# Kernel optimization log

Hardware: AMD Instinct MI355X
Metric: run time of the kernel (lower is better)

Reference implementation:

```python
import jax, jax.numpy as jnp
import numpy as np

B, S, D, H = 2, 2048, 1024, 16
HD = D // H  # head_dim = 64


def setup_inputs() -> dict:
    key = jax.random.key(0)
    ks = jax.random.split(key, 5)
    scale = 1.0 / np.sqrt(D)
    return {
        "x": jax.random.normal(ks[0], (B, S, D), dtype=jnp.float32),
        "attention_mask": jnp.zeros((B, 1, 1, S), dtype=jnp.float32),
        "Wq": jax.random.normal(ks[1], (D, D), dtype=jnp.float32) * scale,
        "Wk": jax.random.normal(ks[2], (D, D), dtype=jnp.float32) * scale,
        "Wv": jax.random.normal(ks[3], (D, D), dtype=jnp.float32) * scale,
        "Wo": jax.random.normal(ks[4], (D, D), dtype=jnp.float32) * scale,
    }


def reference(x, attention_mask, Wq, Wk, Wv, Wo):
    # nn.Linear applies x @ W.T; weights here stored as [out, in]
    q = jnp.einsum("bsd,ed->bse", x, Wq).reshape(B, S, H, HD).transpose(0, 2, 1, 3)
    k = jnp.einsum("bsd,ed->bse", x, Wk).reshape(B, S, H, HD).transpose(0, 2, 1, 3)
    v = jnp.einsum("bsd,ed->bse", x, Wv).reshape(B, S, H, HD).transpose(0, 2, 1, 3)
    scores = jnp.einsum("bhqd,bhkd->bhqk", q, k) / jnp.sqrt(jnp.float32(HD))
    scores = scores + attention_mask  # additive mask, broadcasts [B,1,1,S]
    attn = jax.nn.softmax(scores, axis=-1)  # dropout p=0 (eval) -> identity
    ctx = jnp.einsum("bhqk,bhkd->bhqd", attn, v)
    ctx = ctx.transpose(0, 2, 1, 3).reshape(B, S, D)
    out = jnp.einsum("bsd,ed->bse", ctx, Wo)
    return out
```

## Files before the change

kernel.cpp:

```cpp
#include <hip/hip_runtime.h>
#include <hip/hip_bf16.h>
#include <cstdint>
#include <cstddef>


#define B_  2
#define S_  2048
#define D_  1024
#define H_  16
#define HD_ 64

typedef __bf16 bf16x8 __attribute__((ext_vector_type(8)));
typedef __bf16 bf16x4 __attribute__((ext_vector_type(4)));
typedef float  f32x4  __attribute__((ext_vector_type(4)));

__device__ __forceinline__ void async16(const __bf16* g, const __bf16* l) {
  __builtin_amdgcn_global_load_lds(
      (const __attribute__((address_space(1))) void*)(uintptr_t)g,
      (__attribute__((address_space(3))) void*)(uint32_t)(uintptr_t)l,
      16, 0, 0);
}

__global__ __launch_bounds__(256) void cvt_all(const float* __restrict__ x,
    const float* __restrict__ wq, const float* __restrict__ wk,
    const float* __restrict__ wv, const float* __restrict__ wo,
    __bf16* __restrict__ xb, __bf16* __restrict__ wqb, __bf16* __restrict__ wkb,
    __bf16* __restrict__ wvb, __bf16* __restrict__ wob) {
  const int sel = blockIdx.y;
  const float* src; __bf16* dst; int n;
  if      (sel == 0) { src = x;  dst = xb;  n = B_ * S_ * D_; }
  else if (sel == 1) { src = wq; dst = wqb; n = D_ * D_; }
  else if (sel == 2) { src = wk; dst = wkb; n = D_ * D_; }
  else if (sel == 3) { src = wv; dst = wvb; n = D_ * D_; }
  else               { src = wo; dst = wob; n = D_ * D_; }
  for (int i = blockIdx.x * 256 + threadIdx.x; i * 4 < n; i += gridDim.x * 256) {
    const float4 v = *(const float4*)(src + (size_t)i * 4);
    bf16x4 o;
    o[0] = (__bf16)v.x; o[1] = (__bf16)v.y; o[2] = (__bf16)v.z; o[3] = (__bf16)v.w;
    *(bf16x4*)(dst + (size_t)i * 4) = o;
  }
}

template <typename TC>
__device__ __forceinline__ void gemm97_body(const __bf16* __restrict__ A,
                                            const __bf16* __restrict__ Bm,
                                            TC* __restrict__ C,
                                            const int m0, const int n0,
                                            const int N, const int K) {
  __shared__ __align__(16) __bf16 As[128 * 64];
  __shared__ __align__(16) __bf16 Bs[128 * 64];
  const int tid  = threadIdx.x, lane = tid & 63, wave = tid >> 6;
  const int l15  = lane & 15,   quad = lane >> 4;
  const int wr   = wave >> 1,   wc   = wave & 1;
  const int ebase = wave * 2048 + lane * 8;

  f32x4 acc[4][4] = {};
  for (int k0 = 0; k0 < K; k0 += 64) {
#pragma unroll
    for (int i = 0; i < 4; ++i) {
      const int e = ebase + i * 512;
      const int row = e >> 6, col = e & 63;
      async16(A  + (size_t)(m0 + row) * K + k0 + col, As + (wave * 4 + i) * 512);
      async16(Bm + (size_t)(n0 + row) * K + k0 + col, Bs + (wave * 4 + i) * 512);
    }
    __syncthreads();
#pragma unroll
    for (int kk = 0; kk < 2; ++kk) {
      bf16x8 af[4], bfv[4];
#pragma unroll
      for (int rt = 0; rt < 4; ++rt)
        af[rt] = *(const bf16x8*)(As + (wr * 64 + rt * 16 + l15) * 64 + kk * 32 + quad * 8);
#pragma unroll
      for (int ct = 0; ct < 4; ++ct)
        bfv[ct] = *(const bf16x8*)(Bs + (wc * 64 + ct * 16 + l15) * 64 + kk * 32 + quad * 8);
#pragma unroll
      for (int rt = 0; rt < 4; ++rt)
#pragma unroll
        for (int ct = 0; ct < 4; ++ct)
          acc[rt][ct] = __builtin_amdgcn_mfma_f32_16x16x32_bf16(af[rt], bfv[ct], acc[rt][ct], 0, 0, 0);
    }
    __syncthreads();
  }
#pragma unroll
  for (int rt = 0; rt < 4; ++rt)
#pragma unroll
    for (int ct = 0; ct < 4; ++ct)
#pragma unroll
      for (int r = 0; r < 4; ++r) {
        const int row = m0 + wr * 64 + rt * 16 + quad * 4 + r;
        const int col = n0 + wc * 64 + ct * 16 + l15;
        C[(size_t)row * N + col] = (TC)acc[rt][ct][r];
      }
}

__global__ __launch_bounds__(256) void qkv_gemm(const __bf16* __restrict__ xb,
                                                const __bf16* __restrict__ wq,
                                                const __bf16* __restrict__ wk,
                                                const __bf16* __restrict__ wv,
                                                __bf16* __restrict__ qkv) {
  const int sel = blockIdx.x >> 3;
  const __bf16* Bm = (sel == 0) ? wq : (sel == 1) ? wk : wv;
  __bf16* C = qkv + (size_t)sel * ((size_t)B_ * S_ * D_);
  gemm97_body<__bf16>(xb, Bm, C, blockIdx.y * 128, (blockIdx.x & 7) * 128, D_, D_);
}

__global__ __launch_bounds__(256) void o_gemm(const __bf16* __restrict__ cb,
                                              const __bf16* __restrict__ wo,
                                              float* __restrict__ out) {
  gemm97_body<float>(cb, wo, out, blockIdx.y * 128, blockIdx.x * 128, D_, D_);
}

__global__ __launch_bounds__(256) void vtrans(const __bf16* __restrict__ vb,
                                              __bf16* __restrict__ vt) {
  __shared__ __bf16 tbuf[64][72];
  const int tid = threadIdx.x;
  const int s0 = blockIdx.x * 64, bh = blockIdx.y;
  const int b = bh >> 4, h = bh & 15;
  const __bf16* src = vb + ((size_t)b * S_ + s0) * D_ + h * HD_;
#pragma unroll
  for (int i = 0; i < 2; ++i) {
    const int r = i * 32 + (tid >> 3), c8 = (tid & 7) * 8;
    *(bf16x8*)(&tbuf[r][c8]) = *(const bf16x8*)(src + (size_t)r * D_ + c8);
  }
  __syncthreads();
  __bf16* dst = vt + (size_t)bh * HD_ * S_ + s0;
#pragma unroll
  for (int i = 0; i < 2; ++i) {
    const int hd = i * 32 + (tid >> 3), sc = (tid & 7) * 8;
    bf16x8 v;
#pragma unroll
    for (int j = 0; j < 8; ++j) v[j] = tbuf[sc + j][hd];
    *(bf16x8*)(dst + (size_t)hd * S_ + sc) = v;
  }
}

__global__ __launch_bounds__(256) void attn2(const __bf16* __restrict__ Q,
                                             const __bf16* __restrict__ K,
                                             const __bf16* __restrict__ Vt,
                                             const float* __restrict__ mask,
                                             __bf16* __restrict__ O) {
  constexpr int LKT = 72, LVT = 136, LPS = 136;
  __shared__ __align__(16) __bf16 kt[128 * LKT];
  __shared__ __align__(16) __bf16 vt[64 * LVT];
  __shared__ __align__(16) __bf16 ps[128 * LPS];
  __shared__ __align__(16) float  msk[128];

  const int tid  = threadIdx.x, lane = tid & 63, wave = tid >> 6;
  const int l15  = lane & 15,   quad = lane >> 4;
  const int b = blockIdx.z, h = blockIdx.y, q0 = blockIdx.x * 128;
  const size_t base   = (size_t)b * S_ * D_ + h * HD_;
  const size_t vtbase = (size_t)(b * H_ + h) * HD_ * S_;
  const int qw = q0 + wave * 32;

  bf16x8 qf[2][2];
#pragma unroll
  for (int t = 0; t < 2; ++t)
#pragma unroll
    for (int kb = 0; kb < 2; ++kb)
      qf[t][kb] = *(const bf16x8*)(Q + base + (size_t)(qw + t * 16 + l15) * D_ + kb * 32 + quad * 8);

  float m_run[2] = {-1e30f, -1e30f}, l_run[2] = {0.f, 0.f};
  f32x4 oacc[2][4] = {};

  for (int t0 = 0; t0 < S_; t0 += 128) {
    __syncthreads();
#pragma unroll
    for (int i = 0; i < 4; ++i) {
      const int idx = i * 256 + tid;
      { const int row = idx >> 3, c8 = (idx & 7) * 8;
        *(bf16x8*)(kt + row * LKT + c8) =
            *(const bf16x8*)(K + base + (size_t)(t0 + row) * D_ + c8); }
      { const int row = idx >> 4, c8 = (idx & 15) * 8;
        *(bf16x8*)(vt + row * LVT + c8) =
            *(const bf16x8*)(Vt + vtbase + (size_t)row * S_ + t0 + c8); }
    }
    if (tid < 128) msk[tid] = mask[(size_t)b * S_ + t0 + tid];
    __syncthreads();

    f32x4 sacc[8][2] = {};
#pragma unroll
    for (int kti = 0; kti < 8; ++kti) {
      const __bf16* kr = kt + (kti * 16 + l15) * LKT + quad * 8;
      const bf16x8 a0 = *(const bf16x8*)(kr);
      const bf16x8 a1 = *(const bf16x8*)(kr + 32);
#pragma unroll
      for (int t = 0; t < 2; ++t) {
        sacc[kti][t] = __builtin_amdgcn_mfma_f32_16x16x32_bf16(a0, qf[t][0], sacc[kti][t], 0, 0, 0);
        sacc[kti][t] = __builtin_amdgcn_mfma_f32_16x16x32_bf16(a1, qf[t][1], sacc[kti][t], 0, 0, 0);
      }
    }
#pragma unroll
    for (int kti = 0; kti < 8; ++kti) {
      const f32x4 mv = *(const f32x4*)(msk + kti * 16 + quad * 4);
#pragma unroll
      for (int t = 0; t < 2; ++t)
#pragma unroll
        for (int r = 0; r < 4; ++r)
          sacc[kti][t][r] = sacc[kti][t][r] * 0.125f + mv[r];
    }
    float mnew[2], alpha[2], tsum[2];
#pragma unroll
    for (int t = 0; t < 2; ++t) {
      float tm = -1e30f;
#pragma unroll
      for (int kti = 0; kti < 8; ++kti)
#pragma unroll
        for (int r = 0; r < 4; ++r) tm = fmaxf(tm, sacc[kti][t][r]);
      tm = fmaxf(tm, __shfl_xor(tm, 16));
      tm = fmaxf(tm, __shfl_xor(tm, 32));
      mnew[t]  = fmaxf(m_run[t], tm);
      alpha[t] = __expf(m_run[t] - mnew[t]);
      m_run[t] = mnew[t];
      tsum[t]  = 0.f;
    }
#pragma unroll
    for (int t = 0; t < 2; ++t) {
      __bf16* pr = ps + (size_t)(wave * 32 + t * 16 + l15) * LPS + quad * 4;
#pragma unroll
      for (int kti = 0; kti < 8; ++kti) {
        bf16x4 pv;
#pragma unroll
        for (int r = 0; r < 4; ++r) {
          const float p = __expf(sacc[kti][t][r] - mnew[t]);
          tsum[t] += p;
          pv[r] = (__bf16)p;
        }
        *(bf16x4*)(pr + kti * 16) = pv;
      }
    }
#pragma unroll
    for (int t = 0; t < 2; ++t) {
      float ts = tsum[t];
      ts += __shfl_xor(ts, 16);
      ts += __shfl_xor(ts, 32);
      l_run[t] = l_run[t] * alpha[t] + ts;
#pragma unroll
      for (int r = 0; r < 4; ++r) {
        const float aR = __shfl(alpha[t], quad * 4 + r);
#pragma unroll
        for (int nt = 0; nt < 4; ++nt) oacc[t][nt][r] *= aR;
      }
    }
#pragma unroll
    for (int kb = 0; kb < 4; ++kb) {
      bf16x8 pa[2];
#pragma unroll
      for (int t = 0; t < 2; ++t)
        pa[t] = *(const bf16x8*)(ps + (size_t)(wave * 32 + t * 16 + l15) * LPS + kb * 32 + quad * 8);
#pragma unroll
      for (int nt = 0; nt < 4; ++nt) {
        const bf16x8 vf = *(const bf16x8*)(vt + (nt * 16 + l15) * LVT + kb * 32 + quad * 8);
#pragma unroll
        for (int t = 0; t < 2; ++t)
          oacc[t][nt] = __builtin_amdgcn_mfma_f32_16x16x32_bf16(pa[t], vf, oacc[t][nt], 0, 0, 0);
      }
    }
  }
#pragma unroll
  for (int t = 0; t < 2; ++t)
#pragma unroll
    for (int r = 0; r < 4; ++r) {
      const float lR  = __shfl(l_run[t], quad * 4 + r);
      const float inv = 1.0f / lR;
      const int row = qw + t * 16 + quad * 4 + r;
#pragma unroll
      for (int nt = 0; nt < 4; ++nt)
        O[base + (size_t)row * D_ + nt * 16 + l15] = (__bf16)(oacc[t][nt][r] * inv);
    }
}

extern "C" void kernel_launch(void* const* d_in, const int* in_sizes, int n_in,
                              void* d_out, int out_size, void* d_ws, size_t ws_size,
                              hipStream_t stream) {
  const float* x    = (const float*)d_in[0];
  const float* mask = (const float*)d_in[1];
  const float* Wq   = (const float*)d_in[2];
  const float* Wk   = (const float*)d_in[3];
  const float* Wv   = (const float*)d_in[4];
  const float* Wo   = (const float*)d_in[5];

  char* ws = (char*)d_ws;
  const size_t MB = 1ull << 20;
  const size_t NT = (size_t)B_ * S_ * D_;
  __bf16* xb  = (__bf16*)(ws);
  __bf16* wqb = (__bf16*)(ws + 8 * MB);
  __bf16* wkb = (__bf16*)(ws + 10 * MB);
  __bf16* wvb = (__bf16*)(ws + 12 * MB);
  __bf16* wob = (__bf16*)(ws + 14 * MB);
  __bf16* qkv = (__bf16*)(ws + 16 * MB);
  __bf16* qb  = qkv;
  __bf16* kb  = qkv + NT;
  __bf16* vb  = qkv + 2 * NT;
  __bf16* vtb = xb;
  __bf16* cb  = vb;

  cvt_all<<<dim3(1024, 5), 256, 0, stream>>>(x, Wq, Wk, Wv, Wo, xb, wqb, wkb, wvb, wob);
  qkv_gemm<<<dim3(24, 32), 256, 0, stream>>>(xb, wqb, wkb, wvb, qkv);
  vtrans<<<dim3(32, 32), 256, 0, stream>>>(vb, vtb);
  attn2<<<dim3(S_ / 128, H_, B_), 256, 0, stream>>>(qb, kb, vtb, mask, cb);
  o_gemm<<<dim3(8, 32), 256, 0, stream>>>(cb, wob, (float*)d_out);
}
```

Baseline: 232.4 us.

## Rework attention kernel: 8 waves, register-resident P, exp2 softmax, lazy rescale

The attention kernel now runs 512 threads, each wave owning 16 query rows instead of 32, with launch bounds requesting higher occupancy. The probability tile no longer goes through shared memory: it is packed to bf16 with v_cvt_pk_bf16_f32 and rearranged across lanes with permlane swaps so it can feed the PV MFMA directly from registers. Softmax now uses exp2 with log2e folded into the scale and the mask. The running max is only updated and the accumulator only rescaled when a new max exceeds the old one by more than a threshold. MFMA blocks are wrapped in s_setprio. Together these aim to cut LDS traffic, barrier pressure and exp/rescale ALU work, at the cost of more register-level lane shuffling and a looser but still exact-normalised max handling.

```diff
diff --git a/kernel.cpp b/kernel.cpp
--- a/kernel.cpp
+++ b/kernel.cpp
@@ -19,6 +19,12 @@
       (const __attribute__((address_space(1))) void*)(uintptr_t)g,
       (__attribute__((address_space(3))) void*)(uint32_t)(uintptr_t)l,
       16, 0, 0);
+}
+
+__device__ __forceinline__ unsigned cvt_pk_bf16(float lo, float hi) {
+  unsigned r;
+  asm("v_cvt_pk_bf16_f32 %0, %1, %2" : "=v"(r) : "v"(lo), "v"(hi));
+  return r;
 }
 
 __global__ __launch_bounds__(256) void cvt_all(const float* __restrict__ x,
@@ -134,15 +140,14 @@
   }
 }
 
-__global__ __launch_bounds__(256) void attn2(const __bf16* __restrict__ Q,
-                                             const __bf16* __restrict__ K,
-                                             const __bf16* __restrict__ Vt,
-                                             const float* __restrict__ mask,
-                                             __bf16* __restrict__ O) {
-  constexpr int LKT = 72, LVT = 136, LPS = 136;
+__global__ __launch_bounds__(512, 4) void attn2(const __bf16* __restrict__ Q,
+                                                const __bf16* __restrict__ K,
+                                                const __bf16* __restrict__ Vt,
+                                                const float* __restrict__ mask,
+                                                __bf16* __restrict__ O) {
+  constexpr int LKT = 72, LVT = 136;
   __shared__ __align__(16) __bf16 kt[128 * LKT];
   __shared__ __align__(16) __bf16 vt[64 * LVT];
-  __shared__ __align__(16) __bf16 ps[128 * LPS];
   __shared__ __align__(16) float  msk[128];
 
   const int tid  = threadIdx.x, lane = tid & 63, wave = tid >> 6;
@@ -150,23 +155,23 @@
   const int b = blockIdx.z, h = blockIdx.y, q0 = blockIdx.x * 128;
   const size_t base   = (size_t)b * S_ * D_ + h * HD_;
   const size_t vtbase = (size_t)(b * H_ + h) * HD_ * S_;
-  const int qw = q0 + wave * 32;
-
-  bf16x8 qf[2][2];
-#pragma unroll
-  for (int t = 0; t < 2; ++t)
-#pragma unroll
-    for (int kb = 0; kb < 2; ++kb)
-      qf[t][kb] = *(const bf16x8*)(Q + base + (size_t)(qw + t * 16 + l15) * D_ + kb * 32 + quad * 8);
-
-  float m_run[2] = {-1e30f, -1e30f}, l_run[2] = {0.f, 0.f};
-  f32x4 oacc[2][4] = {};
+  const int qw = q0 + wave * 16;
+  constexpr float LOG2E = 1.44269504088896340736f;
+  constexpr float SC    = 0.125f * LOG2E;
+
+  bf16x8 qf[2];
+#pragma unroll
+  for (int kb = 0; kb < 2; ++kb)
+    qf[kb] = *(const bf16x8*)(Q + base + (size_t)(qw + l15) * D_ + kb * 32 + quad * 8);
+
+  float m_run = -1e30f, l_run = 0.f;
+  f32x4 oacc[4] = {};
 
   for (int t0 = 0; t0 < S_; t0 += 128) {
     __syncthreads();
 #pragma unroll
-    for (int i = 0; i < 4; ++i) {
-      const int idx = i * 256 + tid;
+    for (int i = 0; i < 2; ++i) {
+      const int idx = i * 512 + tid;
       { const int row = idx >> 3, c8 = (idx & 7) * 8;
         *(bf16x8*)(kt + row * LKT + c8) =
             *(const bf16x8*)(K + base + (size_t)(t0 + row) * D_ + c8); }
@@ -174,99 +179,96 @@
         *(bf16x8*)(vt + row * LVT + c8) =
             *(const bf16x8*)(Vt + vtbase + (size_t)row * S_ + t0 + c8); }
     }
-    if (tid < 128) msk[tid] = mask[(size_t)b * S_ + t0 + tid];
+    if (tid < 128) msk[tid] = mask[(size_t)b * S_ + t0 + tid] * LOG2E;
     __syncthreads();
 
-    f32x4 sacc[8][2] = {};
+    f32x4 sacc[8] = {};
+    __builtin_amdgcn_s_setprio(1);
 #pragma unroll
     for (int kti = 0; kti < 8; ++kti) {
       const __bf16* kr = kt + (kti * 16 + l15) * LKT + quad * 8;
       const bf16x8 a0 = *(const bf16x8*)(kr);
       const bf16x8 a1 = *(const bf16x8*)(kr + 32);
-#pragma unroll
-      for (int t = 0; t < 2; ++t) {
-        sacc[kti][t] = __builtin_amdgcn_mfma_f32_16x16x32_bf16(a0, qf[t][0], sacc[kti][t], 0, 0, 0);
-        sacc[kti][t] = __builtin_amdgcn_mfma_f32_16x16x32_bf16(a1, qf[t][1], sacc[kti][t], 0, 0, 0);
-      }
-    }
+      sacc[kti] = __builtin_amdgcn_mfma_f32_16x16x32_bf16(a0, qf[0], sacc[kti], 0, 0, 0);
+      sacc[kti] = __builtin_amdgcn_mfma_f32_16x16x32_bf16(a1, qf[1], sacc[kti], 0, 0, 0);
+    }
+    __builtin_amdgcn_s_setprio(0);
+
+    f32x4 tm4;
+#pragma unroll
+    for (int r = 0; r < 4; ++r) tm4[r] = -1e30f;
 #pragma unroll
     for (int kti = 0; kti < 8; ++kti) {
       const f32x4 mv = *(const f32x4*)(msk + kti * 16 + quad * 4);
 #pragma unroll
-      for (int t = 0; t < 2; ++t)
-#pragma unroll
-        for (int r = 0; r < 4; ++r)
-          sacc[kti][t][r] = sacc[kti][t][r] * 0.125f + mv[r];
-    }
-    float mnew[2], alpha[2], tsum[2];
-#pragma unroll
-    for (int t = 0; t < 2; ++t) {
-      float tm = -1e30f;
-#pragma unroll
-      for (int kti = 0; kti < 8; ++kti)
-#pragma unroll
-        for (int r = 0; r < 4; ++r) tm = fmaxf(tm, sacc[kti][t][r]);
-      tm = fmaxf(tm, __shfl_xor(tm, 16));
-      tm = fmaxf(tm, __shfl_xor(tm, 32));
-      mnew[t]  = fmaxf(m_run[t], tm);
-      alpha[t] = __expf(m_run[t] - mnew[t]);
-      m_run[t] = mnew[t];
-      tsum[t]  = 0.f;
-    }
-#pragma unroll
-    for (int t = 0; t < 2; ++t) {
-      __bf16* pr = ps + (size_t)(wave * 32 + t * 16 + l15) * LPS + quad * 4;
-#pragma unroll
-      for (int kti = 0; kti < 8; ++kti) {
-        bf16x4 pv;
+      for (int r = 0; r < 4; ++r) {
+        sacc[kti][r] = sacc[kti][r] * SC + mv[r];
+        tm4[r] = fmaxf(tm4[r], sacc[kti][r]);
+      }
+    }
+    float tm = fmaxf(fmaxf(tm4[0], tm4[1]), fmaxf(tm4[2], tm4[3]));
+    tm = fmaxf(tm, __shfl_xor(tm, 16));
+    tm = fmaxf(tm, __shfl_xor(tm, 32));
+
+    if (!__all(tm <= m_run + 8.f)) {
+      const float mnew  = fmaxf(m_run, tm);
+      const float alpha = __builtin_amdgcn_exp2f(m_run - mnew);
+      m_run = mnew;
+      l_run *= alpha;
+#pragma unroll
+      for (int r = 0; r < 4; ++r) {
+        const float aR = __shfl(alpha, quad * 4 + r);
+#pragma unroll
+        for (int nt = 0; nt < 4; ++nt) oacc[nt][r] *= aR;
+      }
+    }
+
+    float ts = 0.f;
+#pragma unroll
+    for (int kb = 0; kb < 4; ++kb) {
+      unsigned dd[2][2];
+#pragma unroll
+      for (int kk = 0; kk < 2; ++kk) {
+        const int kti = 2 * kb + kk;
+        float p[4];
 #pragma unroll
         for (int r = 0; r < 4; ++r) {
-          const float p = __expf(sacc[kti][t][r] - mnew[t]);
-          tsum[t] += p;
-          pv[r] = (__bf16)p;
+          p[r] = __builtin_amdgcn_exp2f(sacc[kti][r] - m_run);
+          ts += p[r];
         }
-        *(bf16x4*)(pr + kti * 16) = pv;
-      }
-    }
-#pragma unroll
-    for (int t = 0; t < 2; ++t) {
-      float ts = tsum[t];
-      ts += __shfl_xor(ts, 16);
-      ts += __shfl_xor(ts, 32);
-      l_run[t] = l_run[t] * alpha[t] + ts;
-#pragma unroll
-      for (int r = 0; r < 4; ++r) {
-        const float aR = __shfl(alpha[t], quad * 4 + r);
-#pragma unroll
-        for (int nt = 0; nt < 4; ++nt) oacc[t][nt][r] *= aR;
-      }
-    }
-#pragma unroll
-    for (int kb = 0; kb < 4; ++kb) {
-      bf16x8 pa[2];
-#pragma unroll
-      for (int t = 0; t < 2; ++t)
-        pa[t] = *(const bf16x8*)(ps + (size_t)(wave * 32 + t * 16 + l15) * LPS + kb * 32 + quad * 8);
+        dd[kk][0] = cvt_pk_bf16(p[0], p[1]);
+        dd[kk][1] = cvt_pk_bf16(p[2], p[3]);
+      }
+      unsigned a0 = dd[0][0], b0 = dd[1][0], a1 = dd[0][1], b1 = dd[1][1];
+      asm("v_permlane32_swap_b32 %0, %1" : "+v"(a0), "+v"(b0));
+      asm("v_permlane16_swap_b32 %0, %1" : "+v"(a0), "+v"(b0));
+      asm("v_permlane32_swap_b32 %0, %1" : "+v"(a1), "+v"(b1));
+      asm("v_permlane16_swap_b32 %0, %1" : "+v"(a1), "+v"(b1));
+      union { unsigned u[4]; bf16x8 v; } pw;
+      pw.u[0] = a0; pw.u[1] = a1; pw.u[2] = b0; pw.u[3] = b1;
+      const bf16x8 pa = pw.v;
+      __builtin_amdgcn_s_setprio(1);
 #pragma unroll
       for (int nt = 0; nt < 4; ++nt) {
         const bf16x8 vf = *(const bf16x8*)(vt + (nt * 16 + l15) * LVT + kb * 32 + quad * 8);
-#pragma unroll
-        for (int t = 0; t < 2; ++t)
-          oacc[t][nt] = __builtin_amdgcn_mfma_f32_16x16x32_bf16(pa[t], vf, oacc[t][nt], 0, 0, 0);
-      }
-    }
-  }
-#pragma unroll
-  for (int t = 0; t < 2; ++t)
-#pragma unroll
-    for (int r = 0; r < 4; ++r) {
-      const float lR  = __shfl(l_run[t], quad * 4 + r);
-      const float inv = 1.0f / lR;
-      const int row = qw + t * 16 + quad * 4 + r;
-#pragma unroll
-      for (int nt = 0; nt < 4; ++nt)
-        O[base + (size_t)row * D_ + nt * 16 + l15] = (__bf16)(oacc[t][nt][r] * inv);
-    }
+        oacc[nt] = __builtin_amdgcn_mfma_f32_16x16x32_bf16(pa, vf, oacc[nt], 0, 0, 0);
+      }
+      __builtin_amdgcn_s_setprio(0);
+    }
+    ts += __shfl_xor(ts, 16);
+    ts += __shfl_xor(ts, 32);
+    l_run += ts;
+  }
+
+#pragma unroll
+  for (int r = 0; r < 4; ++r) {
+    const float lR  = __shfl(l_run, quad * 4 + r);
+    const float inv = 1.0f / lR;
+    const int row = qw + quad * 4 + r;
+#pragma unroll
+    for (int nt = 0; nt < 4; ++nt)
+      O[base + (size_t)row * D_ + nt * 16 + l15] = (__bf16)(oacc[nt][r] * inv);
+  }
 }
 
 extern "C" void kernel_launch(void* const* d_in, const int* in_sizes, int n_in,
@@ -297,6 +299,6 @@
   cvt_all<<<dim3(1024, 5), 256, 0, stream>>>(x, Wq, Wk, Wv, Wo, xb, wqb, wkb, wvb, wob);
   qkv_gemm<<<dim3(24, 32), 256, 0, stream>>>(xb, wqb, wkb, wvb, qkv);
   vtrans<<<dim3(32, 32), 256, 0, stream>>>(vb, vtb);
-  attn2<<<dim3(S_ / 128, H_, B_), 256, 0, stream>>>(qb, kb, vtb, mask, cb);
+  attn2<<<dim3(S_ / 128, H_, B_), 512, 0, stream>>>(qb, kb, vtb, mask, cb);
   o_gemm<<<dim3(8, 32), 256, 0, stream>>>(cb, wob, (float*)d_out);
 }
```

Measured after the change: 226.9 us. 2.4% less time.
